# Optimization experiments

Measured on AMD Instinct MI355X. Metric: run time of the kernel, lower is better.

The kernel has to match this reference:

```python
import jax, jax.numpy as jnp
import numpy as np

B, C, CI, H, W = 8, 64, 64, 256, 256  # in_channels=64, inter_channels=64, square H=W required by the module's reshapes


def conv1x1(x, w, b):
    # x: [B,Cin,H,W], w: [Cout,Cin], b: [Cout]
    return jnp.einsum('bchw,oc->bohw', x, w) + b[None, :, None, None]


def setup_inputs() -> dict:
    key = jax.random.key(0)
    ks = jax.random.split(key, 10)
    s_in = 1.0 / np.sqrt(C)
    s_int = 1.0 / np.sqrt(CI)
    return {
        'x': jax.random.normal(ks[0], (B, C, H, W), jnp.float32),
        'ref': jax.random.normal(ks[1], (B, C, H, W), jnp.float32),
        'w_g': jax.random.normal(ks[2], (CI, C), jnp.float32) * s_in,
        'b_g': jax.random.normal(ks[3], (CI,), jnp.float32) * s_in,
        'w_theta': jax.random.normal(ks[4], (CI, C), jnp.float32) * s_in,
        'b_theta': jax.random.normal(ks[5], (CI,), jnp.float32) * s_in,
        'w_phi': jax.random.normal(ks[6], (CI, C), jnp.float32) * s_in,
        'b_phi': jax.random.normal(ks[7], (CI,), jnp.float32) * s_in,
        'w_W': jax.random.normal(ks[8], (C, CI), jnp.float32) * s_int,
        'b_W': jax.random.normal(ks[9], (C,), jnp.float32) * s_int,
    }


def reference(x, ref, w_g, b_g, w_theta, b_theta, w_phi, b_phi, w_W, b_W):
    b = x.shape[0]
    h = x.shape[2]
    # 1x1 conv projections then raw row-major reshape [B,Ci,H,W] -> [B, H, Ci*W]
    # (matches torch .view on contiguous NCHW: mixes channel and height indices)
    g_x = conv1x1(x, w_g, b_g).reshape(b, h, -1)          # [B,H,Ci*W]
    theta_x = conv1x1(ref, w_theta, b_theta).reshape(b, h, -1)
    phi_x = conv1x1(x, w_phi, b_phi).reshape(b, h, -1)
    # attention over height: f = theta @ phi^T, softmax over dim=1 (rows, per column)
    f = jnp.einsum('bif,bjf->bij', theta_x, phi_x)        # [B,H,H]
    f_div_C = jax.nn.softmax(f, axis=1)
    y = jnp.einsum('bij,bjf->bif', f_div_C, g_x)          # [B,H,Ci*W]
    y = jnp.transpose(y, (0, 2, 1)).reshape(b, x.shape[1], x.shape[2], h)  # [B,C,H,H]
    W_y = conv1x1(y, w_W, b_W)
    return W_y + x
```

## Files before the change

### kernel.cpp

```cpp
#include <hip/hip_runtime.h>
#include <hip/hip_bf16.h>

#define B_   8
#define C_   64
#define H_   256
#define W_   256
#define HW_  65536
#define CHW  4194304
#define F_   16384
#define KSPLIT 16
#define KCH  1024

typedef __attribute__((ext_vector_type(8)))  short  short8;
typedef __attribute__((ext_vector_type(4)))  float  floatx4;

__device__ __forceinline__ unsigned short f2bf(float v) {
    unsigned int u = __builtin_bit_cast(unsigned int, v);
    unsigned int r = u + 0x7fffu + ((u >> 16) & 1u);
    return (unsigned short)(r >> 16);
}
__device__ __forceinline__ float bf2f(unsigned short h) {
    unsigned int u = ((unsigned int)h) << 16;
    return __builtin_bit_cast(float, u);
}


__global__ __launch_bounds__(256) void prep_kernel(
    const float* __restrict__ w_phi, const float* __restrict__ w_g,
    const float* __restrict__ w_theta, const float* __restrict__ w_W,
    float* __restrict__ wt4)
{
    int tid = threadIdx.x;
    const float* src[4] = {w_phi, w_g, w_theta, w_W};
#pragma unroll
    for (int m = 0; m < 4; ++m) {
        float* dst = wt4 + m * 4096;
        const float* s = src[m];
#pragma unroll
        for (int r = 0; r < 16; ++r) {
            int idx = r * 256 + tid;
            int o = idx >> 6, c = idx & 63;
            dst[c * 64 + o] = s[idx];
        }
    }
}

template<bool HASRES>
__device__ __forceinline__ void g64_pass(
    const float (*sX)[132], const float (*sW)[68],
    int tp, int to, const float* __restrict__ bias,
    const float* __restrict__ resid, float* __restrict__ outp, size_t base)
{
    float4 acc[8];
#pragma unroll
    for (int i = 0; i < 8; ++i) acc[i] = (float4){0.f, 0.f, 0.f, 0.f};
#pragma unroll 8
    for (int k = 0; k < 64; ++k) {
        float4 xv = *(const float4*)&sX[k][tp * 4];
        float4 w0 = *(const float4*)&sW[k][to * 4];
        float4 w1 = *(const float4*)&sW[k][32 + to * 4];
        float wv[8] = {w0.x, w0.y, w0.z, w0.w, w1.x, w1.y, w1.z, w1.w};
#pragma unroll
        for (int oo = 0; oo < 8; ++oo) {
            acc[oo].x = fmaf(wv[oo], xv.x, acc[oo].x);
            acc[oo].y = fmaf(wv[oo], xv.y, acc[oo].y);
            acc[oo].z = fmaf(wv[oo], xv.z, acc[oo].z);
            acc[oo].w = fmaf(wv[oo], xv.w, acc[oo].w);
        }
    }
#pragma unroll
    for (int oo = 0; oo < 8; ++oo) {
        int o = (oo < 4) ? (to * 4 + oo) : (32 + to * 4 + (oo - 4));
        float bv = bias[o];
        size_t ob = base + (size_t)o * HW_ + tp * 4;
        float4 v = {acc[oo].x + bv, acc[oo].y + bv, acc[oo].z + bv, acc[oo].w + bv};
        if (HASRES) {
            float4 r = *(const float4*)&resid[ob];
            v.x += r.x; v.y += r.y; v.z += r.z; v.w += r.w;
        }
        *(float4*)&outp[ob] = v;
    }
}

__global__ __launch_bounds__(256) void g64x3_kernel(
    const float* __restrict__ x, const float* __restrict__ ref,
    const float* __restrict__ wt4,
    const float* __restrict__ b_p, const float* __restrict__ b_g,
    const float* __restrict__ b_t,
    float* __restrict__ phi, float* __restrict__ gout,
    float* __restrict__ theta)
{
    __shared__ float sX[64][132];
    __shared__ float sW[64][68];
    int blk = blockIdx.x;
    int b  = blk >> 9;
    int p0 = (blk & 511) << 7;
    size_t base = (size_t)b * CHW + p0;
    int tid  = threadIdx.x;
    int tp   = tid & 31;
    int to   = tid >> 5;
    int srow = tid >> 4;
    int scol = (tid & 15) * 8;
    int wrow = tid >> 2;
    int wcol = (tid & 3) * 16;

#pragma unroll
    for (int q = 0; q < 4; ++q) {
        int c = srow + q * 16;
        const float* sp = &x[base + (size_t)c * HW_ + scol];
        *(float4*)&sX[c][scol]     = *(const float4*)sp;
        *(float4*)&sX[c][scol + 4] = *(const float4*)(sp + 4);
    }
#pragma unroll
    for (int q = 0; q < 4; ++q)
        *(float4*)&sW[wrow][wcol + q * 4] = *(const float4*)&wt4[wrow * 64 + wcol + q * 4];
    __syncthreads();
    g64_pass<false>(sX, sW, tp, to, b_p, nullptr, phi, base);
    __syncthreads();
#pragma unroll
    for (int q = 0; q < 4; ++q)
        *(float4*)&sW[wrow][wcol + q * 4] = *(const float4*)&wt4[4096 + wrow * 64 + wcol + q * 4];
    __syncthreads();
    g64_pass<false>(sX, sW, tp, to, b_g, nullptr, gout, base);
    __syncthreads();
#pragma unroll
    for (int q = 0; q < 4; ++q) {
        int c = srow + q * 16;
        const float* sp = &ref[base + (size_t)c * HW_ + scol];
        *(float4*)&sX[c][scol]     = *(const float4*)sp;
        *(float4*)&sX[c][scol + 4] = *(const float4*)(sp + 4);
    }
#pragma unroll
    for (int q = 0; q < 4; ++q)
        *(float4*)&sW[wrow][wcol + q * 4] = *(const float4*)&wt4[8192 + wrow * 64 + wcol + q * 4];
    __syncthreads();
    g64_pass<false>(sX, sW, tp, to, b_t, nullptr, theta, base);
}

__global__ __launch_bounds__(256) void g64f_kernel(
    const float* __restrict__ yt, const float* __restrict__ wtW,
    const float* __restrict__ bW, const float* __restrict__ resid,
    float* __restrict__ out)
{
    __shared__ float sX[64][132];
    __shared__ float sW[64][68];
    int blk = blockIdx.x;
    int b  = blk >> 9;
    int p0 = (blk & 511) << 7;
    size_t base = (size_t)b * CHW + p0;
    int tid  = threadIdx.x;
    int tp   = tid & 31;
    int to   = tid >> 5;
    int srow = tid >> 4;
    int scol = (tid & 15) * 8;
    int wrow = tid >> 2;
    int wcol = (tid & 3) * 16;

#pragma unroll
    for (int q = 0; q < 4; ++q) {
        int c = srow + q * 16;
        const float* sp = &yt[base + (size_t)c * HW_ + scol];
        *(float4*)&sX[c][scol]     = *(const float4*)sp;
        *(float4*)&sX[c][scol + 4] = *(const float4*)(sp + 4);
    }
#pragma unroll
    for (int q = 0; q < 4; ++q)
        *(float4*)&sW[wrow][wcol + q * 4] = *(const float4*)&wtW[wrow * 64 + wcol + q * 4];
    __syncthreads();
    g64_pass<true>(sX, sW, tp, to, bW, resid, out, base);
}

#define FST 40
__global__ __launch_bounds__(256) void fmat_kernel(
    const float* __restrict__ theta, const float* __restrict__ phi,
    float* __restrict__ fpart)
{
    __shared__ unsigned short sPh[128 * FST];
    __shared__ unsigned short sPl[128 * FST];
    __shared__ unsigned short sTh[128 * FST];
    __shared__ unsigned short sTl[128 * FST];

    int blk = blockIdx.x;
    int ks = blk & 15;
    int it = (blk >> 4) & 1;
    int jt = (blk >> 5) & 1;
    int b  = blk >> 6;
    int k0 = ks * KCH;
    int i0 = it * 128, j0 = jt * 128;
    const float* phiB = phi   + (size_t)b * CHW + (size_t)j0 * F_ + k0;
    const float* theB = theta + (size_t)b * CHW + (size_t)i0 * F_ + k0;

    int tid  = threadIdx.x;
    int wave = tid >> 6;
    int lane = tid & 63;
    int wj = wave >> 1, wi = wave & 1;
    int frow = lane & 15;
    int fkq  = lane >> 4;

    int sr = tid >> 2;
    int sk = (tid & 3) * 4;

    floatx4 acc[4][4];
#pragma unroll
    for (int a = 0; a < 4; ++a)
#pragma unroll
        for (int q = 0; q < 4; ++q) acc[a][q] = (floatx4){0.f, 0.f, 0.f, 0.f};

    for (int kk = 0; kk < KCH; kk += 32) {
        float4 pv[4], tv[4];
#pragma unroll
        for (int q = 0; q < 4; ++q) {
            int row = sr + (q & 1) * 64;
            int ko  = sk + (q >> 1) * 16;
            pv[q] = *(const float4*)&phiB[(size_t)row * F_ + kk + ko];
            tv[q] = *(const float4*)&theB[(size_t)row * F_ + kk + ko];
        }
        __syncthreads();
#pragma unroll
        for (int q = 0; q < 4; ++q) {
            int row = sr + (q & 1) * 64;
            int ko  = sk + (q >> 1) * 16;
            int idx = row * FST + ko;
            float pf[4] = {pv[q].x, pv[q].y, pv[q].z, pv[q].w};
            float tf[4] = {tv[q].x, tv[q].y, tv[q].z, tv[q].w};
            ushort4 ph, pl, th, tl;
            unsigned short* php = (unsigned short*)&ph;
            unsigned short* plp = (unsigned short*)&pl;
            unsigned short* thp = (unsigned short*)&th;
            unsigned short* tlp = (unsigned short*)&tl;
#pragma unroll
            for (int e = 0; e < 4; ++e) {
                unsigned short h = f2bf(pf[e]);
                php[e] = h;
                plp[e] = f2bf(pf[e] - bf2f(h));
                h = f2bf(tf[e]);
                thp[e] = h;
                tlp[e] = f2bf(tf[e] - bf2f(h));
            }
            *(ushort4*)&sPh[idx] = ph;
            *(ushort4*)&sPl[idx] = pl;
            *(ushort4*)&sTh[idx] = th;
            *(ushort4*)&sTl[idx] = tl;
        }
        __syncthreads();

        short8 bh[4], bl[4];
#pragma unroll
        for (int ii = 0; ii < 4; ++ii) {
            int ridx = (wi * 64 + ii * 16 + frow) * FST + fkq * 8;
            bh[ii] = *(const short8*)&sTh[ridx];
            bl[ii] = *(const short8*)&sTl[ridx];
        }
#pragma unroll
        for (int jj = 0; jj < 4; ++jj) {
            int ridx = (wj * 64 + jj * 16 + frow) * FST + fkq * 8;
            short8 ah = *(const short8*)&sPh[ridx];
            short8 al = *(const short8*)&sPl[ridx];
#pragma unroll
            for (int ii = 0; ii < 4; ++ii) {
                acc[jj][ii] = __builtin_amdgcn_mfma_f32_16x16x32_bf16(ah, bh[ii], acc[jj][ii], 0, 0, 0);
                acc[jj][ii] = __builtin_amdgcn_mfma_f32_16x16x32_bf16(ah, bl[ii], acc[jj][ii], 0, 0, 0);
                acc[jj][ii] = __builtin_amdgcn_mfma_f32_16x16x32_bf16(al, bh[ii], acc[jj][ii], 0, 0, 0);
            }
        }
    }

    size_t obase = (size_t)(b * KSPLIT + ks) * 65536;
#pragma unroll
    for (int jj = 0; jj < 4; ++jj) {
#pragma unroll
        for (int ii = 0; ii < 4; ++ii) {
            int i = i0 + wi * 64 + ii * 16 + frow;
#pragma unroll
            for (int r = 0; r < 4; ++r) {
                int j = j0 + wj * 64 + jj * 16 + fkq * 4 + r;
                fpart[obase + (size_t)j * 256 + i] = acc[jj][ii][r];
            }
        }
    }
}

__global__ __launch_bounds__(256) void softmax_kernel(
    const float* __restrict__ fpart,
    unsigned short* __restrict__ AtTh,
    unsigned short* __restrict__ AtTl)
{
    __shared__ float red[8];
    int blk = blockIdx.x;
    int b = blk >> 8, j = blk & 255;
    int i = threadIdx.x;
    float v = 0.f;
#pragma unroll
    for (int ks = 0; ks < KSPLIT; ++ks)
        v += fpart[(size_t)(b * KSPLIT + ks) * 65536 + (size_t)j * 256 + i];
    float m = v;
#pragma unroll
    for (int off = 32; off >= 1; off >>= 1) m = fmaxf(m, __shfl_xor(m, off, 64));
    if ((i & 63) == 0) red[i >> 6] = m;
    __syncthreads();
    m = fmaxf(fmaxf(red[0], red[1]), fmaxf(red[2], red[3]));
    float e = __expf(v - m);
    float s = e;
#pragma unroll
    for (int off = 32; off >= 1; off >>= 1) s += __shfl_xor(s, off, 64);
    if ((i & 63) == 0) red[4 + (i >> 6)] = s;
    __syncthreads();
    s = red[4] + red[5] + red[6] + red[7];
    float a = e / s;
    unsigned short h = f2bf(a);
    unsigned short l = f2bf(a - bf2f(h));
    size_t o = (size_t)b * 65536 + (size_t)i * 256 + j;
    AtTh[o] = h;
    AtTl[o] = l;
}

__global__ __launch_bounds__(256) void ymat_kernel(
    const float* __restrict__ g,
    const unsigned short* __restrict__ AtTh,
    const unsigned short* __restrict__ AtTl,
    float* __restrict__ yt)
{
    __shared__ __attribute__((aligned(16))) unsigned short sGh[128 * 40];
    __shared__ __attribute__((aligned(16))) unsigned short sGl[128 * 40];
    __shared__ __attribute__((aligned(16))) unsigned short sAh[128 * 40];
    __shared__ __attribute__((aligned(16))) unsigned short sAl[128 * 40];

    int blk = blockIdx.x;
    int it = blk & 1;
    int Ft = (blk >> 1) & 127;
    int b  = blk >> 8;
    int F0 = Ft * 128;
    int i0 = it * 128;
    const float* gB = g + (size_t)b * CHW + F0;
    const unsigned short* ahB = AtTh + (size_t)b * 65536 + (size_t)i0 * 256;
    const unsigned short* alB = AtTl + (size_t)b * 65536 + (size_t)i0 * 256;

    int tid  = threadIdx.x;
    int wave = tid >> 6;
    int lane = tid & 63;
    int wj = wave >> 1, wi = wave & 1;
    int frow = lane & 15;
    int fkq  = lane >> 4;

    int fq = tid & 31;
    int jq = tid >> 5;
    int ail = tid >> 1;
    int ahf = (tid & 1) * 16;

    floatx4 acc[4][4];
#pragma unroll
    for (int a = 0; a < 4; ++a)
#pragma unroll
        for (int q = 0; q < 4; ++q) acc[a][q] = (floatx4){0.f, 0.f, 0.f, 0.f};

    for (int kk = 0; kk < 256; kk += 32) {
        float4 gv[4];
#pragma unroll
        for (int d = 0; d < 4; ++d)
            gv[d] = *(const float4*)&gB[(size_t)(kk + jq * 4 + d) * F_ + fq * 4];
        short8 a0h = *(const short8*)&ahB[(size_t)ail * 256 + kk + ahf];
        short8 a1h = *(const short8*)&ahB[(size_t)ail * 256 + kk + ahf + 8];
        short8 a0l = *(const short8*)&alB[(size_t)ail * 256 + kk + ahf];
        short8 a1l = *(const short8*)&alB[(size_t)ail * 256 + kk + ahf + 8];
        __syncthreads();

        *(short8*)&sAh[ail * 40 + ahf]     = a0h;
        *(short8*)&sAh[ail * 40 + ahf + 8] = a1h;
        *(short8*)&sAl[ail * 40 + ahf]     = a0l;
        *(short8*)&sAl[ail * 40 + ahf + 8] = a1l;

#pragma unroll
        for (int e = 0; e < 4; ++e) {
            ushort4 hq, lq;
            unsigned short* hp = (unsigned short*)&hq;
            unsigned short* lp = (unsigned short*)&lq;
#pragma unroll
            for (int d = 0; d < 4; ++d) {
                float v = ((const float*)&gv[d])[e];
                unsigned short h = f2bf(v);
                hp[d] = h;
                lp[d] = f2bf(v - bf2f(h));
            }
            int f = fq * 4 + e;
            int off = f * 40 + ((((jq >> 1) ^ (f >> 2)) & 3) << 3) + (jq & 1) * 4;
            *(ushort4*)&sGh[off] = hq;
            *(ushort4*)&sGl[off] = lq;
        }
        __syncthreads();

        short8 bh[4], bl[4];
#pragma unroll
        for (int ii = 0; ii < 4; ++ii) {
            int ridx = (wi * 64 + ii * 16 + frow) * 40 + fkq * 8;
            bh[ii] = *(const short8*)&sAh[ridx];
            bl[ii] = *(const short8*)&sAl[ridx];
        }
#pragma unroll
        for (int jj = 0; jj < 4; ++jj) {
            int f = wj * 64 + jj * 16 + frow;
            int ridx = f * 40 + (((fkq ^ (f >> 2)) & 3) << 3);
            short8 ah = *(const short8*)&sGh[ridx];
            short8 al = *(const short8*)&sGl[ridx];
#pragma unroll
            for (int ii = 0; ii < 4; ++ii) {
                acc[jj][ii] = __builtin_amdgcn_mfma_f32_16x16x32_bf16(ah, bh[ii], acc[jj][ii], 0, 0, 0);
                acc[jj][ii] = __builtin_amdgcn_mfma_f32_16x16x32_bf16(ah, bl[ii], acc[jj][ii], 0, 0, 0);
                acc[jj][ii] = __builtin_amdgcn_mfma_f32_16x16x32_bf16(al, bh[ii], acc[jj][ii], 0, 0, 0);
            }
        }
    }

    size_t ybase = (size_t)b * CHW;
#pragma unroll
    for (int jj = 0; jj < 4; ++jj) {
#pragma unroll
        for (int ii = 0; ii < 4; ++ii) {
            int ig = i0 + wi * 64 + ii * 16 + frow;
#pragma unroll
            for (int r = 0; r < 4; ++r) {
                int Fg = F0 + wj * 64 + jj * 16 + fkq * 4 + r;
                yt[ybase + (size_t)Fg * 256 + ig] = acc[jj][ii][r];
            }
        }
    }
}

extern "C" void kernel_launch(void* const* d_in, const int* in_sizes, int n_in,
                              void* d_out, int out_size, void* d_ws, size_t ws_size,
                              hipStream_t stream) {
    const float* x   = (const float*)d_in[0];
    const float* ref = (const float*)d_in[1];
    const float* w_g = (const float*)d_in[2];
    const float* b_g = (const float*)d_in[3];
    const float* w_t = (const float*)d_in[4];
    const float* b_t = (const float*)d_in[5];
    const float* w_p = (const float*)d_in[6];
    const float* b_p = (const float*)d_in[7];
    const float* w_W = (const float*)d_in[8];
    const float* b_W = (const float*)d_in[9];
    float* out = (float*)d_out;
    float* ws  = (float*)d_ws;

    float* theta = ws;
    float* phi   = ws + 33554432;
    float* g     = ws + 67108864;
    float* yt    = ws;
    float* fpart = ws + 100663296;
    float* wt4   = ws + 109051904;
    unsigned short* AtTh = (unsigned short*)(ws + 33554432);
    unsigned short* AtTl = AtTh + 524288;

    prep_kernel<<<1, 256, 0, stream>>>(w_p, w_g, w_t, w_W, wt4);
    g64x3_kernel<<<4096, 256, 0, stream>>>(x, ref, wt4, b_p, b_g, b_t,
                                           phi, g, theta);
    fmat_kernel<<<512, 256, 0, stream>>>(theta, phi, fpart);
    softmax_kernel<<<2048, 256, 0, stream>>>(fpart, AtTh, AtTl);
    ymat_kernel<<<2048, 256, 0, stream>>>(g, AtTh, AtTl, yt);
    g64f_kernel<<<4096, 256, 0, stream>>>(yt, wt4 + 12288, b_W, x, out);
}
```

Before: 710.3 us.

## Compute the three 1x1 projections with split-bf16 MFMA instead of FP32 FMA

```diff
diff --git a/kernel.cpp b/kernel.cpp
--- a/kernel.cpp
+++ b/kernel.cpp
@@ -28,20 +28,140 @@
 __global__ __launch_bounds__(256) void prep_kernel(
     const float* __restrict__ w_phi, const float* __restrict__ w_g,
     const float* __restrict__ w_theta, const float* __restrict__ w_W,
-    float* __restrict__ wt4)
+    float* __restrict__ wt4, unsigned short* __restrict__ wf)
 {
     int tid = threadIdx.x;
-    const float* src[4] = {w_phi, w_g, w_theta, w_W};
-#pragma unroll
-    for (int m = 0; m < 4; ++m) {
-        float* dst = wt4 + m * 4096;
-        const float* s = src[m];
-#pragma unroll
-        for (int r = 0; r < 16; ++r) {
-            int idx = r * 256 + tid;
-            int o = idx >> 6, c = idx & 63;
-            dst[c * 64 + o] = s[idx];
-        }
+#pragma unroll
+    for (int r = 0; r < 16; ++r) {
+        int idx = r * 256 + tid;
+        int o = idx >> 6, c = idx & 63;
+        wt4[12288 + c * 64 + o] = w_W[idx];
+    }
+    const float* srcs[3] = {w_phi, w_g, w_theta};
+#pragma unroll
+    for (int p = 0; p < 3; ++p) {
+        const float* w = srcs[p];
+#pragma unroll
+        for (int t = 0; t < 2; ++t) {
+            int s = tid + t * 256;
+            int mi = s >> 7;
+            int ks = (s >> 6) & 1;
+            int lane = s & 63;
+            int frow = lane & 15, fkq = lane >> 4;
+#pragma unroll
+            for (int j = 0; j < 8; ++j) {
+                float v = w[(mi * 16 + frow) * 64 + ks * 32 + fkq * 8 + j];
+                unsigned short h = f2bf(v);
+                wf[p * 8192 + s * 8 + j] = h;
+                wf[p * 8192 + 4096 + s * 8 + j] = f2bf(v - bf2f(h));
+            }
+        }
+    }
+}
+
+__global__ __launch_bounds__(256) void g64x3_kernel(
+    const float* __restrict__ x, const float* __restrict__ ref,
+    const unsigned short* __restrict__ wf,
+    const float* __restrict__ b_p, const float* __restrict__ b_g,
+    const float* __restrict__ b_t,
+    float* __restrict__ phi, float* __restrict__ gout,
+    float* __restrict__ theta)
+{
+    __shared__ __attribute__((aligned(16))) unsigned short sXh[256 * 40];
+    __shared__ __attribute__((aligned(16))) unsigned short sXl[256 * 40];
+
+    int blk = blockIdx.x;
+    int b  = blk >> 8;
+    int px0 = (blk & 255) << 8;
+    size_t bbase = (size_t)b * CHW;
+    size_t base = bbase + px0;
+
+    int tid  = threadIdx.x;
+    int wave = tid >> 6;
+    int lane = tid & 63;
+    int frow = lane & 15;
+    int fkq  = lane >> 4;
+    int o8 = tid >> 6;
+    int q  = tid & 63;
+
+    const float* biases[3] = {b_p, b_g, b_t};
+    float* outs[3] = {phi, gout, theta};
+
+#pragma unroll 1
+    for (int proj = 0; proj < 3; ++proj) {
+        const float* src = (proj == 2) ? ref : x;
+        const unsigned short* wtb = wf + proj * 8192;
+        const float* bias = biases[proj];
+        float* outp = outs[proj];
+
+        floatx4 acc[4][4];
+#pragma unroll
+        for (int a = 0; a < 4; ++a)
+#pragma unroll
+            for (int n = 0; n < 4; ++n) acc[a][n] = (floatx4){0.f, 0.f, 0.f, 0.f};
+
+#pragma unroll 1
+        for (int ks = 0; ks < 2; ++ks) {
+            float4 v[8];
+#pragma unroll
+            for (int d = 0; d < 8; ++d)
+                v[d] = *(const float4*)&src[base + (size_t)(ks * 32 + o8 * 8 + d) * HW_ + q * 4];
+            __syncthreads();
+#pragma unroll
+            for (int e = 0; e < 4; ++e) {
+                short8 hv, lv;
+                unsigned short* hp = (unsigned short*)&hv;
+                unsigned short* lp = (unsigned short*)&lv;
+#pragma unroll
+                for (int d = 0; d < 8; ++d) {
+                    float val = ((const float*)&v[d])[e];
+                    unsigned short h = f2bf(val);
+                    hp[d] = h;
+                    lp[d] = f2bf(val - bf2f(h));
+                }
+                int off = (q * 4 + e) * 40 + o8 * 8;
+                *(short8*)&sXh[off] = hv;
+                *(short8*)&sXl[off] = lv;
+            }
+            __syncthreads();
+
+            short8 bh[4], bl[4];
+#pragma unroll
+            for (int ni = 0; ni < 4; ++ni) {
+                int ridx = (wave * 64 + ni * 16 + frow) * 40 + fkq * 8;
+                bh[ni] = *(const short8*)&sXh[ridx];
+                bl[ni] = *(const short8*)&sXl[ridx];
+            }
+#pragma unroll
+            for (int mi = 0; mi < 4; ++mi) {
+                int widx = ((mi * 2 + ks) * 64 + lane) * 8;
+                short8 ah = *(const short8*)&wtb[widx];
+                short8 al = *(const short8*)&wtb[4096 + widx];
+#pragma unroll
+                for (int ni = 0; ni < 4; ++ni) {
+                    acc[mi][ni] = __builtin_amdgcn_mfma_f32_16x16x32_bf16(ah, bh[ni], acc[mi][ni], 0, 0, 0);
+                    acc[mi][ni] = __builtin_amdgcn_mfma_f32_16x16x32_bf16(ah, bl[ni], acc[mi][ni], 0, 0, 0);
+                    acc[mi][ni] = __builtin_amdgcn_mfma_f32_16x16x32_bf16(al, bh[ni], acc[mi][ni], 0, 0, 0);
+                }
+            }
+        }
+
+#pragma unroll
+        for (int mi = 0; mi < 4; ++mi) {
+            float bv[4];
+#pragma unroll
+            for (int r = 0; r < 4; ++r) bv[r] = bias[mi * 16 + fkq * 4 + r];
+#pragma unroll
+            for (int ni = 0; ni < 4; ++ni) {
+                int px = px0 + wave * 64 + ni * 16 + frow;
+#pragma unroll
+                for (int r = 0; r < 4; ++r) {
+                    int o = mi * 16 + fkq * 4 + r;
+                    outp[bbase + (size_t)o * HW_ + px] = acc[mi][ni][r] + bv[r];
+                }
+            }
+        }
+        __syncthreads();
     }
 }
 
@@ -80,61 +200,6 @@
         }
         *(float4*)&outp[ob] = v;
     }
-}
-
-__global__ __launch_bounds__(256) void g64x3_kernel(
-    const float* __restrict__ x, const float* __restrict__ ref,
-    const float* __restrict__ wt4,
-    const float* __restrict__ b_p, const float* __restrict__ b_g,
-    const float* __restrict__ b_t,
-    float* __restrict__ phi, float* __restrict__ gout,
-    float* __restrict__ theta)
-{
-    __shared__ float sX[64][132];
-    __shared__ float sW[64][68];
-    int blk = blockIdx.x;
-    int b  = blk >> 9;
-    int p0 = (blk & 511) << 7;
-    size_t base = (size_t)b * CHW + p0;
-    int tid  = threadIdx.x;
-    int tp   = tid & 31;
-    int to   = tid >> 5;
-    int srow = tid >> 4;
-    int scol = (tid & 15) * 8;
-    int wrow = tid >> 2;
-    int wcol = (tid & 3) * 16;
-
-#pragma unroll
-    for (int q = 0; q < 4; ++q) {
-        int c = srow + q * 16;
-        const float* sp = &x[base + (size_t)c * HW_ + scol];
-        *(float4*)&sX[c][scol]     = *(const float4*)sp;
-        *(float4*)&sX[c][scol + 4] = *(const float4*)(sp + 4);
-    }
-#pragma unroll
-    for (int q = 0; q < 4; ++q)
-        *(float4*)&sW[wrow][wcol + q * 4] = *(const float4*)&wt4[wrow * 64 + wcol + q * 4];
-    __syncthreads();
-    g64_pass<false>(sX, sW, tp, to, b_p, nullptr, phi, base);
-    __syncthreads();
-#pragma unroll
-    for (int q = 0; q < 4; ++q)
-        *(float4*)&sW[wrow][wcol + q * 4] = *(const float4*)&wt4[4096 + wrow * 64 + wcol + q * 4];
-    __syncthreads();
-    g64_pass<false>(sX, sW, tp, to, b_g, nullptr, gout, base);
-    __syncthreads();
-#pragma unroll
-    for (int q = 0; q < 4; ++q) {
-        int c = srow + q * 16;
-        const float* sp = &ref[base + (size_t)c * HW_ + scol];
-        *(float4*)&sX[c][scol]     = *(const float4*)sp;
-        *(float4*)&sX[c][scol + 4] = *(const float4*)(sp + 4);
-    }
-#pragma unroll
-    for (int q = 0; q < 4; ++q)
-        *(float4*)&sW[wrow][wcol + q * 4] = *(const float4*)&wt4[8192 + wrow * 64 + wcol + q * 4];
-    __syncthreads();
-    g64_pass<false>(sX, sW, tp, to, b_t, nullptr, theta, base);
 }
 
 __global__ __launch_bounds__(256) void g64f_kernel(
@@ -447,11 +512,12 @@
     float* yt    = ws;
     float* fpart = ws + 100663296;
     float* wt4   = ws + 109051904;
+    unsigned short* wf = (unsigned short*)fpart;
     unsigned short* AtTh = (unsigned short*)(ws + 33554432);
     unsigned short* AtTl = AtTh + 524288;
 
-    prep_kernel<<<1, 256, 0, stream>>>(w_p, w_g, w_t, w_W, wt4);
-    g64x3_kernel<<<4096, 256, 0, stream>>>(x, ref, wt4, b_p, b_g, b_t,
+    prep_kernel<<<1, 256, 0, stream>>>(w_p, w_g, w_t, w_W, wt4, wf);
+    g64x3_kernel<<<2048, 256, 0, stream>>>(x, ref, wf, b_p, b_g, b_t,
                                            phi, g, theta);
     fmat_kernel<<<512, 256, 0, stream>>>(theta, phi, fpart);
     softmax_kernel<<<2048, 256, 0, stream>>>(fpart, AtTh, AtTl);
```

After: 677.0 us. 4.7% less time.
